# Kernel tuning notes

Measured on AMD Instinct MI355X. Metric: run time of the kernel, lower is better.

Reference implementation:

```python
import jax, jax.numpy as jnp
import numpy as np

DRUG_NUM, DIS_NUM, HIDE_DIM = 60000, 40000, 128
HOPS, N_LAYERS, N_HEADS, FFN_DIM, N_EDGES = 7, 2, 4, 512, 800000
N_NODES = DRUG_NUM + DIS_NUM


def _ln(x, s, b, eps=1e-5):
    m = jnp.mean(x, axis=-1, keepdims=True)
    v = jnp.var(x, axis=-1, keepdims=True)
    return (x - m) * jax.lax.rsqrt(v + eps) * s + b


def setup_inputs() -> dict:
    ks = jax.random.split(jax.random.key(0), 16)
    L, D, F = N_LAYERS, HIDE_DIM, FFN_DIM
    sd = 0.05  # param init scale
    n = lambda k, shape, s=sd: jax.random.normal(k, shape, jnp.float32) * s
    kk = jax.random.split(ks[15], 12)
    return {
        'ifTraining': 0,
        'uid': jax.random.randint(ks[0], (256,), 0, DRUG_NUM, jnp.int64 if jax.config.jax_enable_x64 else jnp.int32),
        'iid': jax.random.randint(ks[1], (256,), 0, DIS_NUM, jnp.int64 if jax.config.jax_enable_x64 else jnp.int32),
        'norm': 1,
        'drug_emb': n(ks[2], (DRUG_NUM, D), 0.1),
        'dis_emb': n(ks[3], (DIS_NUM, D), 0.1),
        'edge_src': jax.random.randint(ks[4], (N_EDGES,), 0, N_NODES, jnp.int32),
        'edge_dst': jax.random.randint(ks[5], (N_EDGES,), 0, N_NODES, jnp.int32),
        'edge_val': jax.random.uniform(ks[6], (N_EDGES,), jnp.float32) * 0.1,  # normalized adj values
        'att_w': n(ks[7], (D, D)), 'att_b': jnp.zeros((D,), jnp.float32),
        'ln1_s': jnp.ones((L, D), jnp.float32), 'ln1_b': jnp.zeros((L, D), jnp.float32),
        'q_w': n(kk[0], (L, D, D)), 'q_b': jnp.zeros((L, D), jnp.float32),
        'k_w': n(kk[1], (L, D, D)), 'k_b': jnp.zeros((L, D), jnp.float32),
        'v_w': n(kk[2], (L, D, D)), 'v_b': jnp.zeros((L, D), jnp.float32),
        'o_w': n(kk[3], (L, D, D)), 'o_b': jnp.zeros((L, D), jnp.float32),
        'ln2_s': jnp.ones((L, D), jnp.float32), 'ln2_b': jnp.zeros((L, D), jnp.float32),
        'f1_w': n(kk[4], (L, D, F)), 'f1_b': jnp.zeros((L, F), jnp.float32),
        'f2_w': n(kk[5], (L, F, D)), 'f2_b': jnp.zeros((L, D), jnp.float32),
        'fln_s': jnp.ones((D,), jnp.float32), 'fln_b': jnp.zeros((D,), jnp.float32),
        'attn_w': n(kk[6], (2 * D, 1)), 'attn_b': jnp.zeros((1,), jnp.float32),
    }


def reference(ifTraining, uid, iid, norm, drug_emb, dis_emb, edge_src, edge_dst, edge_val,
              att_w, att_b, ln1_s, ln1_b, q_w, q_b, k_w, k_b, v_w, v_b, o_w, o_b,
              ln2_s, ln2_b, f1_w, f1_b, f2_w, f2_b, fln_s, fln_b, attn_w, attn_b):
    N, D, S, dh = N_NODES, HIDE_DIM, HOPS + 1, HIDE_DIM // N_HEADS
    # ---- re_features: K sparse-adjacency hops over concatenated embeddings ----
    x = jnp.concatenate([drug_emb, dis_emb], axis=0)  # [N, D]
    feats = [x]
    for _ in range(HOPS):
        msgs = x[edge_src] * edge_val[:, None]          # [E, D] gather
        x = jax.ops.segment_sum(msgs, edge_dst, num_segments=N)  # [N, D] scatter-add
        feats.append(x)
    nf = jnp.stack(feats, axis=1)                        # [N, S, D]
    # ---- graph-transformer over the hop sequence (eval: dropout = identity) ----
    h = nf @ att_w + att_b                               # [N, S, D]
    for l in range(N_LAYERS):
        y = _ln(h, ln1_s[l], ln1_b[l])
        q = (y @ q_w[l] + q_b[l]).reshape(N, S, N_HEADS, dh)
        k = (y @ k_w[l] + k_b[l]).reshape(N, S, N_HEADS, dh)
        v = (y @ v_w[l] + v_b[l]).reshape(N, S, N_HEADS, dh)
        a = jnp.einsum('nshd,nthd->nhst', q, k) * (dh ** -0.5)
        a = jax.nn.softmax(a, axis=-1)                   # [N, H, S, S]
        y = jnp.einsum('nhst,nthd->nshd', a, v).reshape(N, S, D)
        h = h + (y @ o_w[l] + o_b[l])
        y = _ln(h, ln2_s[l], ln2_b[l])
        h = h + (jax.nn.gelu(y @ f1_w[l] + f1_b[l]) @ f2_w[l] + f2_b[l])
    out = _ln(h, fln_s, fln_b)
    # ---- readout: node token + softmax attention over hop tokens ----
    node = out[:, 0, :]                                  # [N, D]
    neigh = out[:, 1:, :]                                # [N, HOPS, D]
    target = jnp.broadcast_to(node[:, None, :], neigh.shape)
    att = jnp.concatenate([target, neigh], axis=-1) @ attn_w + attn_b  # [N, HOPS, 1]
    att = jax.nn.softmax(att, axis=1)
    final = node + jnp.sum(neigh * att, axis=1)          # [N, D]
    return final[:DRUG_NUM], final[DRUG_NUM:]
```

## Files before the change

### kernel.cpp

```cpp
#include <hip/hip_runtime.h>
#include <hip/hip_bf16.h>

typedef __hip_bfloat16 bf16;
typedef __attribute__((ext_vector_type(8))) short s16x8;
typedef __attribute__((ext_vector_type(4))) float f32x4;

#define NDRUG 60000
#define NDIS  40000
#define NN    100000
#define DIM   128
#define NHOPS 7
#define NEDGE 800000
#define NSB   98

__device__ __forceinline__ float u2f(unsigned short u) {
    union { unsigned int i; float f; } c; c.i = ((unsigned int)u) << 16; return c.f;
}
__device__ __forceinline__ ushort f2u(float f) {
    bf16 h = __float2bfloat16(f);
    return *reinterpret_cast<ushort*>(&h);
}


__global__ void k_init(const float* __restrict__ drug, const float* __restrict__ dis,
                       ushort* __restrict__ nf) {
    int i = blockIdx.x * 256 + threadIdx.x;
    if (i >= NN * 32) return;
    int n = i >> 5, g = (i & 31) << 2;
    const float* sp = (n < NDRUG) ? drug + (size_t)n * 128 + g
                                  : dis + (size_t)(n - NDRUG) * 128 + g;
    float4 v = *(const float4*)sp;
    ushort4 o;
    o.x = f2u(v.x); o.y = f2u(v.y); o.z = f2u(v.z); o.w = f2u(v.w);
    *(ushort4*)(nf + (size_t)n * 1024 + g) = o;
}

__global__ void k_count(const int* __restrict__ edst, int* __restrict__ cnt) {
    int e = blockIdx.x * 256 + threadIdx.x;
    if (e < NEDGE) atomicAdd(&cnt[edst[e]], 1);
}

__global__ void k_scanA(const int* __restrict__ cnt, int* __restrict__ incl,
                        int* __restrict__ btot) {
    __shared__ int part[1024];
    int b = blockIdx.x, t = threadIdx.x;
    int i = b * 1024 + t;
    part[t] = (i < NN) ? cnt[i] : 0;
    __syncthreads();
    for (int o = 1; o < 1024; o <<= 1) {
        int u = (t >= o) ? part[t - o] : 0;
        __syncthreads();
        part[t] += u;
        __syncthreads();
    }
    if (i < NN) incl[i] = part[t];
    if (t == 1023) btot[b] = part[1023];
}

__global__ void k_scanB(const int* __restrict__ btot, int* __restrict__ boff) {
    if (threadIdx.x == 0) {
        int run = 0;
        for (int b = 0; b < NSB; b++) { boff[b] = run; run += btot[b]; }
        boff[NSB] = run;
    }
}

__global__ void k_scanC(const int* __restrict__ cnt, const int* __restrict__ incl,
                        const int* __restrict__ boff, int* __restrict__ rp) {
    int i = blockIdx.x * 256 + threadIdx.x;
    if (i < NN) rp[i] = incl[i] - cnt[i] + boff[i >> 10];
    if (i == 0) rp[NN] = boff[NSB];
}

__global__ void k_copyrp(const int* __restrict__ rp, int* __restrict__ cur) {
    int i = blockIdx.x * 256 + threadIdx.x;
    if (i < NN) cur[i] = rp[i];
}

__global__ void k_scatter(const int* __restrict__ esrc, const int* __restrict__ edst,
                          const float* __restrict__ eval, int* __restrict__ cur,
                          int* __restrict__ ssrc, float* __restrict__ sval) {
    int e = blockIdx.x * 256 + threadIdx.x;
    if (e >= NEDGE) return;
    int d = edst[e];
    int pos = atomicAdd(&cur[d], 1);
    ssrc[pos] = esrc[e];
    sval[pos] = eval[e];
}

__global__ void k_hopg(ushort* __restrict__ nf, const int* __restrict__ rp,
                       const int* __restrict__ ssrc, const float* __restrict__ sval, int s) {
    int t = blockIdx.x * 256 + threadIdx.x;
    if (t >= NN * 32) return;
    int n = t >> 5, d0 = (t & 31) << 2;
    int e0 = rp[n], e1 = rp[n + 1];
    float4 a = make_float4(0.f, 0.f, 0.f, 0.f);
    for (int e = e0; e < e1; e++) {
        int src = ssrc[e];
        float val = sval[e];
        ushort4 u = *(const ushort4*)(nf + (size_t)src * 1024 + (size_t)(s - 1) * 128 + d0);
        a.x += u2f(u.x) * val; a.y += u2f(u.y) * val;
        a.z += u2f(u.z) * val; a.w += u2f(u.w) * val;
    }
    ushort4 o;
    o.x = f2u(a.x); o.y = f2u(a.y); o.z = f2u(a.z); o.w = f2u(a.w);
    *(ushort4*)(nf + (size_t)n * 1024 + (size_t)s * 128 + d0) = o;
}


__global__ void k_pack(const float* __restrict__ W, ushort* __restrict__ P, int K, int Nout) {
    int idx = blockIdx.x * 256 + threadIdx.x;
    int tot = (Nout >> 4) * (K >> 3) * 16;
    if (idx >= tot) return;
    int c = idx & 15;
    int r = idx >> 4;
    int kb = r % (K >> 3);
    int nt = r / (K >> 3);
    ushort o[8];
    #pragma unroll
    for (int i = 0; i < 8; i++)
        o[i] = f2u(W[(size_t)(kb * 8 + i) * Nout + nt * 16 + c]);
    uint4 v;
    v.x = (uint)o[0] | ((uint)o[1] << 16);
    v.y = (uint)o[2] | ((uint)o[3] << 16);
    v.z = (uint)o[4] | ((uint)o[5] << 16);
    v.w = (uint)o[6] | ((uint)o[7] << 16);
    *(uint4*)(P + (size_t)idx * 8) = v;
}

__global__ void k_catb(const float* __restrict__ qb, const float* __restrict__ kb,
                       const float* __restrict__ vb, float* __restrict__ o) {
    int i = threadIdx.x;
    o[i] = (i < 128) ? qb[i] : ((i < 256) ? kb[i - 128] : vb[i - 256]);
}


template <int ACT, int ADD, int OUTBF, int NTPW>
__global__ void k_mgemm(const ushort* __restrict__ X, const ushort* __restrict__ Wp,
                        const float* __restrict__ bias, void* __restrict__ Yv,
                        int M, int K, int Nout) {
    int w = threadIdx.x >> 6, lane = threadIdx.x & 63;
    int lr = lane & 15, lg = lane >> 4;
    int m0 = blockIdx.x * 16;
    int kb8 = K >> 3;
    int row = m0 + lr; if (row > M - 1) row = M - 1;
    const ushort* ap = X + (size_t)row * K + lg * 8;
    f32x4 acc[NTPW] = {};
    for (int k0 = 0; k0 < K; k0 += 32, ap += 32) {
        s16x8 af = *(const s16x8*)ap;
        int kb = (k0 >> 3) + lg;
        #pragma unroll
        for (int t = 0; t < NTPW; t++) {
            int nt = w + t * 4;
            const ushort* bp = Wp + (((size_t)nt * kb8 + kb) * 16 + lr) * 8;
            s16x8 bf_ = *(const s16x8*)bp;
            acc[t] = __builtin_amdgcn_mfma_f32_16x16x32_bf16(af, bf_, acc[t], 0, 0, 0);
        }
    }
    #pragma unroll
    for (int t = 0; t < NTPW; t++) {
        int n = (w + t * 4) * 16 + lr;
        float bv = bias[n];
        #pragma unroll
        for (int j = 0; j < 4; j++) {
            int m = m0 + lg * 4 + j;
            if (m >= M) continue;
            float v = acc[t][j] + bv;
            if (ACT == 1) {
                float x = v;
                float z = 0.7978845608028654f * (x + 0.044715f * x * x * x);
                v = x / (1.0f + __expf(-2.0f * z));
            }
            if (OUTBF) {
                ((ushort*)Yv)[(size_t)m * Nout + n] = f2u(v);
            } else if (ADD) {
                ((float*)Yv)[(size_t)m * Nout + n] += v;
            } else {
                ((float*)Yv)[(size_t)m * Nout + n] = v;
            }
        }
    }
}


__global__ void k_layer(float* __restrict__ H,
                        const ushort* __restrict__ Wqkv, const ushort* __restrict__ Wo,
                        const ushort* __restrict__ Wf1, const ushort* __restrict__ Wf2,
                        const float* __restrict__ s1v, const float* __restrict__ b1v,
                        const float* __restrict__ bqkv, const float* __restrict__ bo,
                        const float* __restrict__ s2v, const float* __restrict__ b2v,
                        const float* __restrict__ bf1, const float* __restrict__ bf2,
                        int M) {
    __shared__ float  h[16][132];
    __shared__ ushort ylds[16][136];
    __shared__ ushort big[16][520];
    __shared__ float  as_[2][256];
    int tid = threadIdx.x;
    int w = tid >> 6, lane = tid & 63;
    int lr = lane & 15, lg = lane >> 4;
    int m0 = blockIdx.x * 16;

    #pragma unroll
    for (int i = 0; i < 2; i++) {
        int gi = i * 256 + tid;
        int row = gi >> 5, c4 = (gi & 31) << 2;
        int grow = m0 + row; if (grow > M - 1) grow = M - 1;
        *(float4*)&h[row][c4] = *(const float4*)(H + (size_t)grow * 128 + c4);
    }
    __syncthreads();

    #pragma unroll
    for (int i = 0; i < 4; i++) {
        int row = w * 4 + i;
        float2 x = *(const float2*)&h[row][lane * 2];
        float sum = x.x + x.y, sq = x.x * x.x + x.y * x.y;
        #pragma unroll
        for (int o = 32; o; o >>= 1) { sum += __shfl_xor(sum, o); sq += __shfl_xor(sq, o); }
        float mean = sum * (1.f / 128.f);
        float inv = rsqrtf(sq * (1.f / 128.f) - mean * mean + 1e-5f);
        float y0 = (x.x - mean) * inv * s1v[lane * 2 + 0] + b1v[lane * 2 + 0];
        float y1 = (x.y - mean) * inv * s1v[lane * 2 + 1] + b1v[lane * 2 + 1];
        *(uint*)&ylds[row][lane * 2] = (uint)f2u(y0) | ((uint)f2u(y1) << 16);
    }
    __syncthreads();

    {
        f32x4 acc[6] = {};
        for (int k0 = 0; k0 < 128; k0 += 32) {
            s16x8 af = *(const s16x8*)&ylds[lr][lg * 8 + k0];
            int kb = (k0 >> 3) + lg;
            #pragma unroll
            for (int t = 0; t < 6; t++) {
                int nt = w + t * 4;
                const ushort* bp = Wqkv + (((size_t)nt * 16 + kb) * 16 + lr) * 8;
                s16x8 bf_ = *(const s16x8*)bp;
                acc[t] = __builtin_amdgcn_mfma_f32_16x16x32_bf16(af, bf_, acc[t], 0, 0, 0);
            }
        }
        #pragma unroll
        for (int t = 0; t < 6; t++) {
            int n = (w + t * 4) * 16 + lr;
            float bv = bqkv[n];
            #pragma unroll
            for (int j = 0; j < 4; j++) big[lg * 4 + j][n] = f2u(acc[t][j] + bv);
        }
    }
    __syncthreads();

    if (w < 2) {
        int hh = lane >> 4, s_ = (lane >> 1) & 7, p = lane & 1;
        const float scale = 0.17677669529663687f;
        float dots[4];
        float mx = -1e30f;
        #pragma unroll
        for (int t4 = 0; t4 < 4; t4++) {
            int t = p * 4 + t4;
            float dot = 0.f;
            #pragma unroll
            for (int d = 0; d < 32; d++)
                dot += u2f(big[w * 8 + s_][hh * 32 + d]) * u2f(big[w * 8 + t][128 + hh * 32 + d]);
            dots[t4] = dot * scale;
            mx = fmaxf(mx, dots[t4]);
        }
        mx = fmaxf(mx, __shfl_xor(mx, 1));
        float sum = 0.f, e4[4];
        #pragma unroll
        for (int t4 = 0; t4 < 4; t4++) { e4[t4] = __expf(dots[t4] - mx); sum += e4[t4]; }
        sum += __shfl_xor(sum, 1);
        float rinv = 1.f / sum;
        #pragma unroll
        for (int t4 = 0; t4 < 4; t4++) as_[w][hh * 64 + s_ * 8 + p * 4 + t4] = e4[t4] * rinv;
    }
    __syncthreads();

    if (w < 2) {
        #pragma unroll
        for (int i = 0; i < 16; i++) {
            int o = i * 64 + lane;
            int ss = o >> 7, rem = o & 127, h2 = rem >> 5, dd = rem & 31;
            float accv = 0.f;
            #pragma unroll
            for (int t = 0; t < 8; t++)
                accv += as_[w][h2 * 64 + ss * 8 + t] * u2f(big[w * 8 + t][256 + h2 * 32 + dd]);
            ylds[w * 8 + ss][rem] = f2u(accv);
        }
    }
    __syncthreads();

    {
        f32x4 acc[2] = {};
        for (int k0 = 0; k0 < 128; k0 += 32) {
            s16x8 af = *(const s16x8*)&ylds[lr][lg * 8 + k0];
            int kb = (k0 >> 3) + lg;
            #pragma unroll
            for (int t = 0; t < 2; t++) {
                int nt = w + t * 4;
                const ushort* bp = Wo + (((size_t)nt * 16 + kb) * 16 + lr) * 8;
                s16x8 bf_ = *(const s16x8*)bp;
                acc[t] = __builtin_amdgcn_mfma_f32_16x16x32_bf16(af, bf_, acc[t], 0, 0, 0);
            }
        }
        #pragma unroll
        for (int t = 0; t < 2; t++) {
            int n = (w + t * 4) * 16 + lr;
            float bv = bo[n];
            #pragma unroll
            for (int j = 0; j < 4; j++) h[lg * 4 + j][n] += acc[t][j] + bv;
        }
    }
    __syncthreads();

    #pragma unroll
    for (int i = 0; i < 4; i++) {
        int row = w * 4 + i;
        float2 x = *(const float2*)&h[row][lane * 2];
        float sum = x.x + x.y, sq = x.x * x.x + x.y * x.y;
        #pragma unroll
        for (int o = 32; o; o >>= 1) { sum += __shfl_xor(sum, o); sq += __shfl_xor(sq, o); }
        float mean = sum * (1.f / 128.f);
        float inv = rsqrtf(sq * (1.f / 128.f) - mean * mean + 1e-5f);
        float y0 = (x.x - mean) * inv * s2v[lane * 2 + 0] + b2v[lane * 2 + 0];
        float y1 = (x.y - mean) * inv * s2v[lane * 2 + 1] + b2v[lane * 2 + 1];
        *(uint*)&ylds[row][lane * 2] = (uint)f2u(y0) | ((uint)f2u(y1) << 16);
    }
    __syncthreads();

    {
        f32x4 acc[8] = {};
        for (int k0 = 0; k0 < 128; k0 += 32) {
            s16x8 af = *(const s16x8*)&ylds[lr][lg * 8 + k0];
            int kb = (k0 >> 3) + lg;
            #pragma unroll
            for (int t = 0; t < 8; t++) {
                int nt = w + t * 4;
                const ushort* bp = Wf1 + (((size_t)nt * 16 + kb) * 16 + lr) * 8;
                s16x8 bf_ = *(const s16x8*)bp;
                acc[t] = __builtin_amdgcn_mfma_f32_16x16x32_bf16(af, bf_, acc[t], 0, 0, 0);
            }
        }
        #pragma unroll
        for (int t = 0; t < 8; t++) {
            int n = (w + t * 4) * 16 + lr;
            float bv = bf1[n];
            #pragma unroll
            for (int j = 0; j < 4; j++) {
                float x = acc[t][j] + bv;
                float z = 0.7978845608028654f * (x + 0.044715f * x * x * x);
                big[lg * 4 + j][n] = f2u(x / (1.0f + __expf(-2.0f * z)));
            }
        }
    }
    __syncthreads();

    {
        f32x4 acc[2] = {};
        for (int k0 = 0; k0 < 512; k0 += 32) {
            s16x8 af = *(const s16x8*)&big[lr][lg * 8 + k0];
            int kb = (k0 >> 3) + lg;
            #pragma unroll
            for (int t = 0; t < 2; t++) {
                int nt = w + t * 4;
                const ushort* bp = Wf2 + (((size_t)nt * 64 + kb) * 16 + lr) * 8;
                s16x8 bf_ = *(const s16x8*)bp;
                acc[t] = __builtin_amdgcn_mfma_f32_16x16x32_bf16(af, bf_, acc[t], 0, 0, 0);
            }
        }
        #pragma unroll
        for (int t = 0; t < 2; t++) {
            int n = (w + t * 4) * 16 + lr;
            float bv = bf2[n];
            #pragma unroll
            for (int j = 0; j < 4; j++) h[lg * 4 + j][n] += acc[t][j] + bv;
        }
    }
    __syncthreads();

    #pragma unroll
    for (int i = 0; i < 2; i++) {
        int gi = i * 256 + tid;
        int row = gi >> 5, c4 = (gi & 31) << 2;
        int grow = m0 + row;
        if (grow < M) *(float4*)(H + (size_t)grow * 128 + c4) = *(const float4*)&h[row][c4];
    }
}


__global__ void k_pool(const float* __restrict__ Hc, const float* __restrict__ fs,
                       const float* __restrict__ fb, const float* __restrict__ aw,
                       const float* __restrict__ ab, float* __restrict__ out,
                       int Nc, int n0g) {
    int w = threadIdx.x >> 6, lane = threadIdx.x & 63;
    int nl = blockIdx.x * 4 + w;
    if (nl >= Nc) return;
    const float* hp = Hc + (size_t)nl * 1024;
    float s0 = fs[lane * 2], s1 = fs[lane * 2 + 1];
    float b0 = fb[lane * 2], b1 = fb[lane * 2 + 1];
    float2 yl[8];
    #pragma unroll
    for (int s = 0; s < 8; s++) {
        float2 x = *(const float2*)(hp + s * DIM + lane * 2);
        float sum = x.x + x.y, sq = x.x * x.x + x.y * x.y;
        #pragma unroll
        for (int o = 32; o; o >>= 1) { sum += __shfl_xor(sum, o); sq += __shfl_xor(sq, o); }
        float mean = sum * (1.f / 128.f);
        float inv = rsqrtf(sq * (1.f / 128.f) - mean * mean + 1e-5f);
        yl[s].x = (x.x - mean) * inv * s0 + b0;
        yl[s].y = (x.y - mean) * inv * s1 + b1;
    }
    float awn0 = aw[lane * 2], awn1 = aw[lane * 2 + 1];
    float awh0 = aw[128 + lane * 2], awh1 = aw[128 + lane * 2 + 1];
    float abv = ab[0];
    float lg[7];
    #pragma unroll
    for (int s = 0; s < 7; s++) {
        float part = yl[0].x * awn0 + yl[0].y * awn1 + yl[s + 1].x * awh0 + yl[s + 1].y * awh1;
        #pragma unroll
        for (int o = 32; o; o >>= 1) part += __shfl_xor(part, o);
        lg[s] = part + abv;
    }
    float mx = lg[0];
    #pragma unroll
    for (int s = 1; s < 7; s++) mx = fmaxf(mx, lg[s]);
    float sum = 0.f;
    #pragma unroll
    for (int s = 0; s < 7; s++) { lg[s] = __expf(lg[s] - mx); sum += lg[s]; }
    float rinv = 1.f / sum;
    float2 f = yl[0];
    #pragma unroll
    for (int s = 0; s < 7; s++) { f.x += lg[s] * rinv * yl[s + 1].x; f.y += lg[s] * rinv * yl[s + 1].y; }
    size_t ob = (size_t)(n0g + nl) * DIM + lane * 2;
    out[ob + 0] = f.x;
    out[ob + 1] = f.y;
}


extern "C" void kernel_launch(void* const* d_in, const int* in_sizes, int n_in,
                              void* d_out, int out_size, void* d_ws, size_t ws_size,
                              hipStream_t stream) {
    const float* drug  = (const float*)d_in[4];
    const float* dis   = (const float*)d_in[5];
    const int*   esrc  = (const int*)d_in[6];
    const int*   edst  = (const int*)d_in[7];
    const float* eval  = (const float*)d_in[8];
    const float* att_w = (const float*)d_in[9];
    const float* att_b = (const float*)d_in[10];
    const float* ln1_s = (const float*)d_in[11];
    const float* ln1_b = (const float*)d_in[12];
    const float* q_w   = (const float*)d_in[13];
    const float* q_b   = (const float*)d_in[14];
    const float* k_w   = (const float*)d_in[15];
    const float* k_b   = (const float*)d_in[16];
    const float* v_w   = (const float*)d_in[17];
    const float* v_b   = (const float*)d_in[18];
    const float* o_w   = (const float*)d_in[19];
    const float* o_b   = (const float*)d_in[20];
    const float* ln2_s = (const float*)d_in[21];
    const float* ln2_b = (const float*)d_in[22];
    const float* f1_w  = (const float*)d_in[23];
    const float* f1_b  = (const float*)d_in[24];
    const float* f2_w  = (const float*)d_in[25];
    const float* f2_b  = (const float*)d_in[26];
    const float* fln_s = (const float*)d_in[27];
    const float* fln_b = (const float*)d_in[28];
    const float* aw    = (const float*)d_in[29];
    const float* ab    = (const float*)d_in[30];
    float* out = (float*)d_out;

    char* ws = (char*)d_ws;
    size_t nfB = (size_t)NN * 1024 * 2;
    ushort* nf = (ushort*)ws;
    size_t off = (nfB + 255) & ~(size_t)255;

    ushort* wpk = (ushort*)(ws + off);
    size_t offCsr = off + (1 << 20);
    int*   rp   = (int*)(ws + offCsr);
    int*   cnt  = rp + (NN + 1);
    int*   ssrc = cnt + NN;
    float* sval = (float*)(ssrc + NEDGE);
    int*   incl = (int*)(sval + NEDGE);
    int*   btot = incl + NN;
    int*   boff = btot + 128;
    size_t csrInts = (size_t)(NN + 1) + NN + NEDGE + NEDGE + NN + 256;
    size_t off2 = offCsr + ((csrInts * 4 + 255) & ~(size_t)255);

    size_t scratchB = (ws_size > off2) ? ws_size - off2 : 0;
    long long ncMax = (long long)(scratchB / 4096);
    ncMax &= ~1LL;
    if (ncMax < 2) ncMax = 2;
    int Nc = (int)((ncMax < NN) ? ncMax : NN);
    int nchunks = (NN + Nc - 1) / Nc;
    Nc = (NN + nchunks - 1) / nchunks;
    if (Nc & 1) Nc++;
    float* hbuf = (float*)(ws + off2);

    size_t wpAtt = 0;
    size_t wpQKV[2], wpO[2], wpF1[2], wpF2[2];
    {
        size_t p = 16384;
        for (int l = 0; l < 2; l++) {
            wpQKV[l] = p; p += 49152;
            wpO[l]   = p; p += 16384;
            wpF1[l]  = p; p += 65536;
            wpF2[l]  = p; p += 65536;
        }
    }
    float* qkvB = (float*)(wpk + 409600);

    {
        int b128 = (16384 / 8 + 255) / 256;
        int b512 = (65536 / 8 + 255) / 256;
        k_pack<<<b128, 256, 0, stream>>>(att_w, wpk + wpAtt, 128, 128);
        for (int l = 0; l < 2; l++) {
            k_pack<<<b128, 256, 0, stream>>>(q_w + (size_t)l * 16384, wpk + wpQKV[l], 128, 128);
            k_pack<<<b128, 256, 0, stream>>>(k_w + (size_t)l * 16384, wpk + wpQKV[l] + 16384, 128, 128);
            k_pack<<<b128, 256, 0, stream>>>(v_w + (size_t)l * 16384, wpk + wpQKV[l] + 32768, 128, 128);
            k_pack<<<b128, 256, 0, stream>>>(o_w + (size_t)l * 16384, wpk + wpO[l], 128, 128);
            k_pack<<<b512, 256, 0, stream>>>(f1_w + (size_t)l * 65536, wpk + wpF1[l], 128, 512);
            k_pack<<<b512, 256, 0, stream>>>(f2_w + (size_t)l * 65536, wpk + wpF2[l], 512, 128);
            k_catb<<<1, 384, 0, stream>>>(q_b + l * 128, k_b + l * 128, v_b + l * 128, qkvB + l * 384);
        }
    }

    (void)hipMemsetAsync(cnt, 0, (size_t)NN * 4, stream);
    k_count<<<(NEDGE + 255) / 256, 256, 0, stream>>>(edst, cnt);
    k_scanA<<<NSB, 1024, 0, stream>>>(cnt, incl, btot);
    k_scanB<<<1, 64, 0, stream>>>(btot, boff);
    k_scanC<<<(NN + 255) / 256, 256, 0, stream>>>(cnt, incl, boff, rp);
    k_copyrp<<<(NN + 255) / 256, 256, 0, stream>>>(rp, cnt);
    k_scatter<<<(NEDGE + 255) / 256, 256, 0, stream>>>(esrc, edst, eval, cnt, ssrc, sval);

    k_init<<<(NN * 32 + 255) / 256, 256, 0, stream>>>(drug, dis, nf);
    for (int s = 1; s <= NHOPS; s++)
        k_hopg<<<(NN * 32 + 255) / 256, 256, 0, stream>>>(nf, rp, ssrc, sval, s);

    for (int c = 0; c < nchunks; c++) {
        int cn0 = c * Nc;
        int cn = NN - cn0; if (cn > Nc) cn = Nc;
        if (cn <= 0) break;
        int Mc = cn * 8;
        int mb = (Mc + 15) / 16;
        int nb = (cn + 3) / 4;

        k_mgemm<0, 0, 0, 2><<<mb, 256, 0, stream>>>(nf + (size_t)cn0 * 1024, wpk + wpAtt,
                                                    att_b, hbuf, Mc, 128, 128);
        for (int l = 0; l < 2; l++) {
            k_layer<<<mb, 256, 0, stream>>>(hbuf, wpk + wpQKV[l], wpk + wpO[l],
                                            wpk + wpF1[l], wpk + wpF2[l],
                                            ln1_s + l * 128, ln1_b + l * 128,
                                            qkvB + l * 384, o_b + l * 128,
                                            ln2_s + l * 128, ln2_b + l * 128,
                                            f1_b + l * 512, f2_b + l * 128, Mc);
        }
        k_pool<<<nb, 256, 0, stream>>>(hbuf, fln_s, fln_b, aw, ab, out, cn, cn0);
    }
    (void)in_sizes; (void)n_in; (void)out_size;
}
```

Baseline: 2.957 ms.

## Fuse both transformer layers into one kernel keeping activations in LDS

Merges the two per-layer k_layer launches into a single k_layer2 kernel that loops over both layers while the 16-row h tile stays in shared memory. This removes one fp32 global write and read of the hidden state per chunk, plus one launch. It also spreads the attention-times-V step across all four waves instead of two. The weight pack offsets are recomputed as fixed layer strides.

```diff
diff --git a/kernel.cpp b/kernel.cpp
--- a/kernel.cpp
+++ b/kernel.cpp
@@ -183,14 +183,13 @@
 }
 
 
-__global__ void k_layer(float* __restrict__ H,
-                        const ushort* __restrict__ Wqkv, const ushort* __restrict__ Wo,
-                        const ushort* __restrict__ Wf1, const ushort* __restrict__ Wf2,
-                        const float* __restrict__ s1v, const float* __restrict__ b1v,
-                        const float* __restrict__ bqkv, const float* __restrict__ bo,
-                        const float* __restrict__ s2v, const float* __restrict__ b2v,
-                        const float* __restrict__ bf1, const float* __restrict__ bf2,
-                        int M) {
+__global__ void k_layer2(float* __restrict__ H, const ushort* __restrict__ wpk,
+                         const float* __restrict__ qkvB,
+                         const float* __restrict__ ln1_s, const float* __restrict__ ln1_b,
+                         const float* __restrict__ o_b,
+                         const float* __restrict__ ln2_s, const float* __restrict__ ln2_b,
+                         const float* __restrict__ f1_b, const float* __restrict__ f2_b,
+                         int M) {
     __shared__ float  h[16][132];
     __shared__ ushort ylds[16][136];
     __shared__ ushort big[16][520];
@@ -209,171 +208,187 @@
     }
     __syncthreads();
 
-    #pragma unroll
-    for (int i = 0; i < 4; i++) {
-        int row = w * 4 + i;
-        float2 x = *(const float2*)&h[row][lane * 2];
-        float sum = x.x + x.y, sq = x.x * x.x + x.y * x.y;
+    for (int l = 0; l < 2; l++) {
+        const ushort* Wqkv = wpk + 16384  + (size_t)l * 196608;
+        const ushort* Wo   = wpk + 65536  + (size_t)l * 196608;
+        const ushort* Wf1  = wpk + 81920  + (size_t)l * 196608;
+        const ushort* Wf2  = wpk + 147456 + (size_t)l * 196608;
+        const float* s1v = ln1_s + l * 128;
+        const float* b1v = ln1_b + l * 128;
+        const float* bqkv = qkvB + l * 384;
+        const float* bo  = o_b + l * 128;
+        const float* s2v = ln2_s + l * 128;
+        const float* b2v = ln2_b + l * 128;
+        const float* bf1 = f1_b + l * 512;
+        const float* bf2 = f2_b + l * 128;
+
         #pragma unroll
-        for (int o = 32; o; o >>= 1) { sum += __shfl_xor(sum, o); sq += __shfl_xor(sq, o); }
-        float mean = sum * (1.f / 128.f);
-        float inv = rsqrtf(sq * (1.f / 128.f) - mean * mean + 1e-5f);
-        float y0 = (x.x - mean) * inv * s1v[lane * 2 + 0] + b1v[lane * 2 + 0];
-        float y1 = (x.y - mean) * inv * s1v[lane * 2 + 1] + b1v[lane * 2 + 1];
-        *(uint*)&ylds[row][lane * 2] = (uint)f2u(y0) | ((uint)f2u(y1) << 16);
-    }
-    __syncthreads();
-
-    {
-        f32x4 acc[6] = {};
-        for (int k0 = 0; k0 < 128; k0 += 32) {
-            s16x8 af = *(const s16x8*)&ylds[lr][lg * 8 + k0];
-            int kb = (k0 >> 3) + lg;
+        for (int i = 0; i < 4; i++) {
+            int row = w * 4 + i;
+            float2 x = *(const float2*)&h[row][lane * 2];
+            float sum = x.x + x.y, sq = x.x * x.x + x.y * x.y;
+            #pragma unroll
+            for (int o = 32; o; o >>= 1) { sum += __shfl_xor(sum, o); sq += __shfl_xor(sq, o); }
+            float mean = sum * (1.f / 128.f);
+            float inv = rsqrtf(sq * (1.f / 128.f) - mean * mean + 1e-5f);
+            float y0 = (x.x - mean) * inv * s1v[lane * 2 + 0] + b1v[lane * 2 + 0];
+            float y1 = (x.y - mean) * inv * s1v[lane * 2 + 1] + b1v[lane * 2 + 1];
+            *(uint*)&ylds[row][lane * 2] = (uint)f2u(y0) | ((uint)f2u(y1) << 16);
+        }
+        __syncthreads();
+
+        {
+            f32x4 acc[6] = {};
+            for (int k0 = 0; k0 < 128; k0 += 32) {
+                s16x8 af = *(const s16x8*)&ylds[lr][lg * 8 + k0];
+                int kb = (k0 >> 3) + lg;
+                #pragma unroll
+                for (int t = 0; t < 6; t++) {
+                    int nt = w + t * 4;
+                    const ushort* bp = Wqkv + (((size_t)nt * 16 + kb) * 16 + lr) * 8;
+                    s16x8 bf_ = *(const s16x8*)bp;
+                    acc[t] = __builtin_amdgcn_mfma_f32_16x16x32_bf16(af, bf_, acc[t], 0, 0, 0);
+                }
+            }
             #pragma unroll
             for (int t = 0; t < 6; t++) {
-                int nt = w + t * 4;
-                const ushort* bp = Wqkv + (((size_t)nt * 16 + kb) * 16 + lr) * 8;
-                s16x8 bf_ = *(const s16x8*)bp;
-                acc[t] = __builtin_amdgcn_mfma_f32_16x16x32_bf16(af, bf_, acc[t], 0, 0, 0);
-            }
-        }
+                int n = (w + t * 4) * 16 + lr;
+                float bv = bqkv[n];
+                #pragma unroll
+                for (int j = 0; j < 4; j++) big[lg * 4 + j][n] = f2u(acc[t][j] + bv);
+            }
+        }
+        __syncthreads();
+
+        if (w < 2) {
+            int hh = lane >> 4, s_ = (lane >> 1) & 7, p = lane & 1;
+            const float scale = 0.17677669529663687f;
+            float dots[4];
+            float mx = -1e30f;
+            #pragma unroll
+            for (int t4 = 0; t4 < 4; t4++) {
+                int t = p * 4 + t4;
+                float dot = 0.f;
+                #pragma unroll
+                for (int d = 0; d < 32; d++)
+                    dot += u2f(big[w * 8 + s_][hh * 32 + d]) * u2f(big[w * 8 + t][128 + hh * 32 + d]);
+                dots[t4] = dot * scale;
+                mx = fmaxf(mx, dots[t4]);
+            }
+            mx = fmaxf(mx, __shfl_xor(mx, 1));
+            float sum = 0.f, e4[4];
+            #pragma unroll
+            for (int t4 = 0; t4 < 4; t4++) { e4[t4] = __expf(dots[t4] - mx); sum += e4[t4]; }
+            sum += __shfl_xor(sum, 1);
+            float rinv = 1.f / sum;
+            #pragma unroll
+            for (int t4 = 0; t4 < 4; t4++) as_[w][hh * 64 + s_ * 8 + p * 4 + t4] = e4[t4] * rinv;
+        }
+        __syncthreads();
+
+        {
+            int nd = w & 1, hf = w >> 1;
+            #pragma unroll
+            for (int i = 0; i < 8; i++) {
+                int o = hf * 512 + i * 64 + lane;
+                int ss = o >> 7, rem = o & 127, h2 = rem >> 5, dd = rem & 31;
+                float accv = 0.f;
+                #pragma unroll
+                for (int t = 0; t < 8; t++)
+                    accv += as_[nd][h2 * 64 + ss * 8 + t] * u2f(big[nd * 8 + t][256 + h2 * 32 + dd]);
+                ylds[nd * 8 + ss][rem] = f2u(accv);
+            }
+        }
+        __syncthreads();
+
+        {
+            f32x4 acc[2] = {};
+            for (int k0 = 0; k0 < 128; k0 += 32) {
+                s16x8 af = *(const s16x8*)&ylds[lr][lg * 8 + k0];
+                int kb = (k0 >> 3) + lg;
+                #pragma unroll
+                for (int t = 0; t < 2; t++) {
+                    int nt = w + t * 4;
+                    const ushort* bp = Wo + (((size_t)nt * 16 + kb) * 16 + lr) * 8;
+                    s16x8 bf_ = *(const s16x8*)bp;
+                    acc[t] = __builtin_amdgcn_mfma_f32_16x16x32_bf16(af, bf_, acc[t], 0, 0, 0);
+                }
+            }
+            #pragma unroll
+            for (int t = 0; t < 2; t++) {
+                int n = (w + t * 4) * 16 + lr;
+                float bv = bo[n];
+                #pragma unroll
+                for (int j = 0; j < 4; j++) h[lg * 4 + j][n] += acc[t][j] + bv;
+            }
+        }
+        __syncthreads();
+
         #pragma unroll
-        for (int t = 0; t < 6; t++) {
-            int n = (w + t * 4) * 16 + lr;
-            float bv = bqkv[n];
-            #pragma unroll
-            for (int j = 0; j < 4; j++) big[lg * 4 + j][n] = f2u(acc[t][j] + bv);
-        }
-    }
-    __syncthreads();
-
-    if (w < 2) {
-        int hh = lane >> 4, s_ = (lane >> 1) & 7, p = lane & 1;
-        const float scale = 0.17677669529663687f;
-        float dots[4];
-        float mx = -1e30f;
-        #pragma unroll
-        for (int t4 = 0; t4 < 4; t4++) {
-            int t = p * 4 + t4;
-            float dot = 0.f;
-            #pragma unroll
-            for (int d = 0; d < 32; d++)
-                dot += u2f(big[w * 8 + s_][hh * 32 + d]) * u2f(big[w * 8 + t][128 + hh * 32 + d]);
-            dots[t4] = dot * scale;
-            mx = fmaxf(mx, dots[t4]);
-        }
-        mx = fmaxf(mx, __shfl_xor(mx, 1));
-        float sum = 0.f, e4[4];
-        #pragma unroll
-        for (int t4 = 0; t4 < 4; t4++) { e4[t4] = __expf(dots[t4] - mx); sum += e4[t4]; }
-        sum += __shfl_xor(sum, 1);
-        float rinv = 1.f / sum;
-        #pragma unroll
-        for (int t4 = 0; t4 < 4; t4++) as_[w][hh * 64 + s_ * 8 + p * 4 + t4] = e4[t4] * rinv;
-    }
-    __syncthreads();
-
-    if (w < 2) {
-        #pragma unroll
-        for (int i = 0; i < 16; i++) {
-            int o = i * 64 + lane;
-            int ss = o >> 7, rem = o & 127, h2 = rem >> 5, dd = rem & 31;
-            float accv = 0.f;
-            #pragma unroll
-            for (int t = 0; t < 8; t++)
-                accv += as_[w][h2 * 64 + ss * 8 + t] * u2f(big[w * 8 + t][256 + h2 * 32 + dd]);
-            ylds[w * 8 + ss][rem] = f2u(accv);
-        }
-    }
-    __syncthreads();
-
-    {
-        f32x4 acc[2] = {};
-        for (int k0 = 0; k0 < 128; k0 += 32) {
-            s16x8 af = *(const s16x8*)&ylds[lr][lg * 8 + k0];
-            int kb = (k0 >> 3) + lg;
+        for (int i = 0; i < 4; i++) {
+            int row = w * 4 + i;
+            float2 x = *(const float2*)&h[row][lane * 2];
+            float sum = x.x + x.y, sq = x.x * x.x + x.y * x.y;
+            #pragma unroll
+            for (int o = 32; o; o >>= 1) { sum += __shfl_xor(sum, o); sq += __shfl_xor(sq, o); }
+            float mean = sum * (1.f / 128.f);
+            float inv = rsqrtf(sq * (1.f / 128.f) - mean * mean + 1e-5f);
+            float y0 = (x.x - mean) * inv * s2v[lane * 2 + 0] + b2v[lane * 2 + 0];
+            float y1 = (x.y - mean) * inv * s2v[lane * 2 + 1] + b2v[lane * 2 + 1];
+            *(uint*)&ylds[row][lane * 2] = (uint)f2u(y0) | ((uint)f2u(y1) << 16);
+        }
+        __syncthreads();
+
+        {
+            f32x4 acc[8] = {};
+            for (int k0 = 0; k0 < 128; k0 += 32) {
+                s16x8 af = *(const s16x8*)&ylds[lr][lg * 8 + k0];
+                int kb = (k0 >> 3) + lg;
+                #pragma unroll
+                for (int t = 0; t < 8; t++) {
+                    int nt = w + t * 4;
+                    const ushort* bp = Wf1 + (((size_t)nt * 16 + kb) * 16 + lr) * 8;
+                    s16x8 bf_ = *(const s16x8*)bp;
+                    acc[t] = __builtin_amdgcn_mfma_f32_16x16x32_bf16(af, bf_, acc[t], 0, 0, 0);
+                }
+            }
+            #pragma unroll
+            for (int t = 0; t < 8; t++) {
+                int n = (w + t * 4) * 16 + lr;
+                float bv = bf1[n];
+                #pragma unroll
+                for (int j = 0; j < 4; j++) {
+                    float x = acc[t][j] + bv;
+                    float z = 0.7978845608028654f * (x + 0.044715f * x * x * x);
+                    big[lg * 4 + j][n] = f2u(x / (1.0f + __expf(-2.0f * z)));
+                }
+            }
+        }
+        __syncthreads();
+
+        {
+            f32x4 acc[2] = {};
+            for (int k0 = 0; k0 < 512; k0 += 32) {
+                s16x8 af = *(const s16x8*)&big[lr][lg * 8 + k0];
+                int kb = (k0 >> 3) + lg;
+                #pragma unroll
+                for (int t = 0; t < 2; t++) {
+                    int nt = w + t * 4;
+                    const ushort* bp = Wf2 + (((size_t)nt * 64 + kb) * 16 + lr) * 8;
+                    s16x8 bf_ = *(const s16x8*)bp;
+                    acc[t] = __builtin_amdgcn_mfma_f32_16x16x32_bf16(af, bf_, acc[t], 0, 0, 0);
+                }
+            }
             #pragma unroll
             for (int t = 0; t < 2; t++) {
-                int nt = w + t * 4;
-                const ushort* bp = Wo + (((size_t)nt * 16 + kb) * 16 + lr) * 8;
-                s16x8 bf_ = *(const s16x8*)bp;
-                acc[t] = __builtin_amdgcn_mfma_f32_16x16x32_bf16(af, bf_, acc[t], 0, 0, 0);
-            }
-        }
-        #pragma unroll
-        for (int t = 0; t < 2; t++) {
-            int n = (w + t * 4) * 16 + lr;
-            float bv = bo[n];
-            #pragma unroll
-            for (int j = 0; j < 4; j++) h[lg * 4 + j][n] += acc[t][j] + bv;
-        }
-    }
-    __syncthreads();
-
-    #pragma unroll
-    for (int i = 0; i < 4; i++) {
-        int row = w * 4 + i;
-        float2 x = *(const float2*)&h[row][lane * 2];
-        float sum = x.x + x.y, sq = x.x * x.x + x.y * x.y;
-        #pragma unroll
-        for (int o = 32; o; o >>= 1) { sum += __shfl_xor(sum, o); sq += __shfl_xor(sq, o); }
-        float mean = sum * (1.f / 128.f);
-        float inv = rsqrtf(sq * (1.f / 128.f) - mean * mean + 1e-5f);
-        float y0 = (x.x - mean) * inv * s2v[lane * 2 + 0] + b2v[lane * 2 + 0];
-        float y1 = (x.y - mean) * inv * s2v[lane * 2 + 1] + b2v[lane * 2 + 1];
-        *(uint*)&ylds[row][lane * 2] = (uint)f2u(y0) | ((uint)f2u(y1) << 16);
-    }
-    __syncthreads();
-
-    {
-        f32x4 acc[8] = {};
-        for (int k0 = 0; k0 < 128; k0 += 32) {
-            s16x8 af = *(const s16x8*)&ylds[lr][lg * 8 + k0];
-            int kb = (k0 >> 3) + lg;
-            #pragma unroll
-            for (int t = 0; t < 8; t++) {
-                int nt = w + t * 4;
-                const ushort* bp = Wf1 + (((size_t)nt * 16 + kb) * 16 + lr) * 8;
-                s16x8 bf_ = *(const s16x8*)bp;
-                acc[t] = __builtin_amdgcn_mfma_f32_16x16x32_bf16(af, bf_, acc[t], 0, 0, 0);
-            }
-        }
-        #pragma unroll
-        for (int t = 0; t < 8; t++) {
-            int n = (w + t * 4) * 16 + lr;
-            float bv = bf1[n];
-            #pragma unroll
-            for (int j = 0; j < 4; j++) {
-                float x = acc[t][j] + bv;
-                float z = 0.7978845608028654f * (x + 0.044715f * x * x * x);
-                big[lg * 4 + j][n] = f2u(x / (1.0f + __expf(-2.0f * z)));
-            }
-        }
-    }
-    __syncthreads();
-
-    {
-        f32x4 acc[2] = {};
-        for (int k0 = 0; k0 < 512; k0 += 32) {
-            s16x8 af = *(const s16x8*)&big[lr][lg * 8 + k0];
-            int kb = (k0 >> 3) + lg;
-            #pragma unroll
-            for (int t = 0; t < 2; t++) {
-                int nt = w + t * 4;
-                const ushort* bp = Wf2 + (((size_t)nt * 64 + kb) * 16 + lr) * 8;
-                s16x8 bf_ = *(const s16x8*)bp;
-                acc[t] = __builtin_amdgcn_mfma_f32_16x16x32_bf16(af, bf_, acc[t], 0, 0, 0);
-            }
-        }
-        #pragma unroll
-        for (int t = 0; t < 2; t++) {
-            int n = (w + t * 4) * 16 + lr;
-            float bv = bf2[n];
-            #pragma unroll
-            for (int j = 0; j < 4; j++) h[lg * 4 + j][n] += acc[t][j] + bv;
-        }
-    }
-    __syncthreads();
+                int n = (w + t * 4) * 16 + lr;
+                float bv = bf2[n];
+                #pragma unroll
+                for (int j = 0; j < 4; j++) h[lg * 4 + j][n] += acc[t][j] + bv;
+            }
+        }
+        __syncthreads();
+    }
 
     #pragma unroll
     for (int i = 0; i < 2; i++) {
@@ -493,30 +508,20 @@
     if (Nc & 1) Nc++;
     float* hbuf = (float*)(ws + off2);
 
-    size_t wpAtt = 0;
-    size_t wpQKV[2], wpO[2], wpF1[2], wpF2[2];
-    {
-        size_t p = 16384;
-        for (int l = 0; l < 2; l++) {
-            wpQKV[l] = p; p += 49152;
-            wpO[l]   = p; p += 16384;
-            wpF1[l]  = p; p += 65536;
-            wpF2[l]  = p; p += 65536;
-        }
-    }
     float* qkvB = (float*)(wpk + 409600);
 
     {
         int b128 = (16384 / 8 + 255) / 256;
         int b512 = (65536 / 8 + 255) / 256;
-        k_pack<<<b128, 256, 0, stream>>>(att_w, wpk + wpAtt, 128, 128);
+        k_pack<<<b128, 256, 0, stream>>>(att_w, wpk, 128, 128);
         for (int l = 0; l < 2; l++) {
-            k_pack<<<b128, 256, 0, stream>>>(q_w + (size_t)l * 16384, wpk + wpQKV[l], 128, 128);
-            k_pack<<<b128, 256, 0, stream>>>(k_w + (size_t)l * 16384, wpk + wpQKV[l] + 16384, 128, 128);
-            k_pack<<<b128, 256, 0, stream>>>(v_w + (size_t)l * 16384, wpk + wpQKV[l] + 32768, 128, 128);
-            k_pack<<<b128, 256, 0, stream>>>(o_w + (size_t)l * 16384, wpk + wpO[l], 128, 128);
-            k_pack<<<b512, 256, 0, stream>>>(f1_w + (size_t)l * 65536, wpk + wpF1[l], 128, 512);
-            k_pack<<<b512, 256, 0, stream>>>(f2_w + (size_t)l * 65536, wpk + wpF2[l], 512, 128);
+            size_t base = 16384 + (size_t)l * 196608;
+            k_pack<<<b128, 256, 0, stream>>>(q_w + (size_t)l * 16384, wpk + base, 128, 128);
+            k_pack<<<b128, 256, 0, stream>>>(k_w + (size_t)l * 16384, wpk + base + 16384, 128, 128);
+            k_pack<<<b128, 256, 0, stream>>>(v_w + (size_t)l * 16384, wpk + base + 32768, 128, 128);
+            k_pack<<<b128, 256, 0, stream>>>(o_w + (size_t)l * 16384, wpk + base + 49152, 128, 128);
+            k_pack<<<b512, 256, 0, stream>>>(f1_w + (size_t)l * 65536, wpk + base + 65536, 128, 512);
+            k_pack<<<b512, 256, 0, stream>>>(f2_w + (size_t)l * 65536, wpk + base + 131072, 512, 128);
             k_catb<<<1, 384, 0, stream>>>(q_b + l * 128, k_b + l * 128, v_b + l * 128, qkvB + l * 384);
         }
     }
@@ -541,16 +546,10 @@
         int mb = (Mc + 15) / 16;
         int nb = (cn + 3) / 4;
 
-        k_mgemm<0, 0, 0, 2><<<mb, 256, 0, stream>>>(nf + (size_t)cn0 * 1024, wpk + wpAtt,
+        k_mgemm<0, 0, 0, 2><<<mb, 256, 0, stream>>>(nf + (size_t)cn0 * 1024, wpk,
                                                     att_b, hbuf, Mc, 128, 128);
-        for (int l = 0; l < 2; l++) {
-            k_layer<<<mb, 256, 0, stream>>>(hbuf, wpk + wpQKV[l], wpk + wpO[l],
-                                            wpk + wpF1[l], wpk + wpF2[l],
-                                            ln1_s + l * 128, ln1_b + l * 128,
-                                            qkvB + l * 384, o_b + l * 128,
-                                            ln2_s + l * 128, ln2_b + l * 128,
-                                            f1_b + l * 512, f2_b + l * 128, Mc);
-        }
+        k_layer2<<<mb, 256, 0, stream>>>(hbuf, wpk, qkvB, ln1_s, ln1_b, o_b,
+                                         ln2_s, ln2_b, f1_b, f2_b, Mc);
         k_pool<<<nb, 256, 0, stream>>>(hbuf, fln_s, fln_b, aw, ab, out, cn, cn0);
     }
     (void)in_sizes; (void)n_in; (void)out_size;
```

Result: slower. 6.587 ms (+122.8%).

## Process 32 rows per block in fused transformer layer kernel

Applied to the files above, without the earlier changes.

The fused layer kernel now handles 32 token rows (4 nodes) per block instead of 16, with each wave issuing two MFMA row fragments that share each loaded weight fragment. Weight traffic from global/L2 per row is halved and all four waves now take part in attention instead of two. The FFN1 stage is split into two passes to limit accumulator register pressure. LDS use per block doubles, which may lower occupancy, and the chunk size is rounded to a multiple of four nodes.

```diff
diff --git a/kernel.cpp b/kernel.cpp
--- a/kernel.cpp
+++ b/kernel.cpp
@@ -191,17 +191,17 @@
                         const float* __restrict__ s2v, const float* __restrict__ b2v,
                         const float* __restrict__ bf1, const float* __restrict__ bf2,
                         int M) {
-    __shared__ float  h[16][132];
-    __shared__ ushort ylds[16][136];
-    __shared__ ushort big[16][520];
-    __shared__ float  as_[2][256];
+    __shared__ float  h[32][132];
+    __shared__ ushort ylds[32][136];
+    __shared__ ushort big[32][520];
+    __shared__ float  as_[4][256];
     int tid = threadIdx.x;
     int w = tid >> 6, lane = tid & 63;
     int lr = lane & 15, lg = lane >> 4;
-    int m0 = blockIdx.x * 16;
-
-    #pragma unroll
-    for (int i = 0; i < 2; i++) {
+    int m0 = blockIdx.x * 32;
+
+    #pragma unroll
+    for (int i = 0; i < 4; i++) {
         int gi = i * 256 + tid;
         int row = gi >> 5, c4 = (gi & 31) << 2;
         int grow = m0 + row; if (grow > M - 1) grow = M - 1;
@@ -210,8 +210,8 @@
     __syncthreads();
 
     #pragma unroll
-    for (int i = 0; i < 4; i++) {
-        int row = w * 4 + i;
+    for (int i = 0; i < 8; i++) {
+        int row = w * 8 + i;
         float2 x = *(const float2*)&h[row][lane * 2];
         float sum = x.x + x.y, sq = x.x * x.x + x.y * x.y;
         #pragma unroll
@@ -225,16 +225,18 @@
     __syncthreads();
 
     {
-        f32x4 acc[6] = {};
+        f32x4 acc[2][6] = {};
         for (int k0 = 0; k0 < 128; k0 += 32) {
-            s16x8 af = *(const s16x8*)&ylds[lr][lg * 8 + k0];
+            s16x8 af0 = *(const s16x8*)&ylds[lr][lg * 8 + k0];
+            s16x8 af1 = *(const s16x8*)&ylds[16 + lr][lg * 8 + k0];
             int kb = (k0 >> 3) + lg;
             #pragma unroll
             for (int t = 0; t < 6; t++) {
                 int nt = w + t * 4;
                 const ushort* bp = Wqkv + (((size_t)nt * 16 + kb) * 16 + lr) * 8;
                 s16x8 bf_ = *(const s16x8*)bp;
-                acc[t] = __builtin_amdgcn_mfma_f32_16x16x32_bf16(af, bf_, acc[t], 0, 0, 0);
+                acc[0][t] = __builtin_amdgcn_mfma_f32_16x16x32_bf16(af0, bf_, acc[0][t], 0, 0, 0);
+                acc[1][t] = __builtin_amdgcn_mfma_f32_16x16x32_bf16(af1, bf_, acc[1][t], 0, 0, 0);
             }
         }
         #pragma unroll
@@ -242,12 +244,15 @@
             int n = (w + t * 4) * 16 + lr;
             float bv = bqkv[n];
             #pragma unroll
-            for (int j = 0; j < 4; j++) big[lg * 4 + j][n] = f2u(acc[t][j] + bv);
-        }
-    }
-    __syncthreads();
-
-    if (w < 2) {
+            for (int rf = 0; rf < 2; rf++)
+                #pragma unroll
+                for (int j = 0; j < 4; j++)
+                    big[rf * 16 + lg * 4 + j][n] = f2u(acc[rf][t][j] + bv);
+        }
+    }
+    __syncthreads();
+
+    {
         int hh = lane >> 4, s_ = (lane >> 1) & 7, p = lane & 1;
         const float scale = 0.17677669529663687f;
         float dots[4];
@@ -273,7 +278,7 @@
     }
     __syncthreads();
 
-    if (w < 2) {
+    {
         #pragma unroll
         for (int i = 0; i < 16; i++) {
             int o = i * 64 + lane;
@@ -288,16 +293,18 @@
     __syncthreads();
 
     {
-        f32x4 acc[2] = {};
+        f32x4 acc[2][2] = {};
         for (int k0 = 0; k0 < 128; k0 += 32) {
-            s16x8 af = *(const s16x8*)&ylds[lr][lg * 8 + k0];
+            s16x8 af0 = *(const s16x8*)&ylds[lr][lg * 8 + k0];
+            s16x8 af1 = *(const s16x8*)&ylds[16 + lr][lg * 8 + k0];
             int kb = (k0 >> 3) + lg;
             #pragma unroll
             for (int t = 0; t < 2; t++) {
                 int nt = w + t * 4;
                 const ushort* bp = Wo + (((size_t)nt * 16 + kb) * 16 + lr) * 8;
                 s16x8 bf_ = *(const s16x8*)bp;
-                acc[t] = __builtin_amdgcn_mfma_f32_16x16x32_bf16(af, bf_, acc[t], 0, 0, 0);
+                acc[0][t] = __builtin_amdgcn_mfma_f32_16x16x32_bf16(af0, bf_, acc[0][t], 0, 0, 0);
+                acc[1][t] = __builtin_amdgcn_mfma_f32_16x16x32_bf16(af1, bf_, acc[1][t], 0, 0, 0);
             }
         }
         #pragma unroll
@@ -305,14 +312,17 @@
             int n = (w + t * 4) * 16 + lr;
             float bv = bo[n];
             #pragma unroll
-            for (int j = 0; j < 4; j++) h[lg * 4 + j][n] += acc[t][j] + bv;
-        }
-    }
-    __syncthreads();
-
-    #pragma unroll
-    for (int i = 0; i < 4; i++) {
-        int row = w * 4 + i;
+            for (int rf = 0; rf < 2; rf++)
+                #pragma unroll
+                for (int j = 0; j < 4; j++)
+                    h[rf * 16 + lg * 4 + j][n] += acc[rf][t][j] + bv;
+        }
+    }
+    __syncthreads();
+
+    #pragma unroll
+    for (int i = 0; i < 8; i++) {
+        int row = w * 8 + i;
         float2 x = *(const float2*)&h[row][lane * 2];
         float sum = x.x + x.y, sq = x.x * x.x + x.y * x.y;
         #pragma unroll
@@ -325,44 +335,51 @@
     }
     __syncthreads();
 
-    {
-        f32x4 acc[8] = {};
+    #pragma unroll
+    for (int ps = 0; ps < 2; ps++) {
+        f32x4 acc[2][4] = {};
         for (int k0 = 0; k0 < 128; k0 += 32) {
-            s16x8 af = *(const s16x8*)&ylds[lr][lg * 8 + k0];
+            s16x8 af0 = *(const s16x8*)&ylds[lr][lg * 8 + k0];
+            s16x8 af1 = *(const s16x8*)&ylds[16 + lr][lg * 8 + k0];
             int kb = (k0 >> 3) + lg;
             #pragma unroll
-            for (int t = 0; t < 8; t++) {
-                int nt = w + t * 4;
+            for (int t = 0; t < 4; t++) {
+                int nt = w + (ps * 4 + t) * 4;
                 const ushort* bp = Wf1 + (((size_t)nt * 16 + kb) * 16 + lr) * 8;
                 s16x8 bf_ = *(const s16x8*)bp;
-                acc[t] = __builtin_amdgcn_mfma_f32_16x16x32_bf16(af, bf_, acc[t], 0, 0, 0);
+                acc[0][t] = __builtin_amdgcn_mfma_f32_16x16x32_bf16(af0, bf_, acc[0][t], 0, 0, 0);
+                acc[1][t] = __builtin_amdgcn_mfma_f32_16x16x32_bf16(af1, bf_, acc[1][t], 0, 0, 0);
             }
         }
         #pragma unroll
-        for (int t = 0; t < 8; t++) {
-            int n = (w + t * 4) * 16 + lr;
+        for (int t = 0; t < 4; t++) {
+            int n = (w + (ps * 4 + t) * 4) * 16 + lr;
             float bv = bf1[n];
             #pragma unroll
-            for (int j = 0; j < 4; j++) {
-                float x = acc[t][j] + bv;
-                float z = 0.7978845608028654f * (x + 0.044715f * x * x * x);
-                big[lg * 4 + j][n] = f2u(x / (1.0f + __expf(-2.0f * z)));
-            }
-        }
-    }
-    __syncthreads();
-
-    {
-        f32x4 acc[2] = {};
+            for (int rf = 0; rf < 2; rf++)
+                #pragma unroll
+                for (int j = 0; j < 4; j++) {
+                    float x = acc[rf][t][j] + bv;
+                    float z = 0.7978845608028654f * (x + 0.044715f * x * x * x);
+                    big[rf * 16 + lg * 4 + j][n] = f2u(x / (1.0f + __expf(-2.0f * z)));
+                }
+        }
+    }
+    __syncthreads();
+
+    {
+        f32x4 acc[2][2] = {};
         for (int k0 = 0; k0 < 512; k0 += 32) {
-            s16x8 af = *(const s16x8*)&big[lr][lg * 8 + k0];
+            s16x8 af0 = *(const s16x8*)&big[lr][lg * 8 + k0];
+            s16x8 af1 = *(const s16x8*)&big[16 + lr][lg * 8 + k0];
             int kb = (k0 >> 3) + lg;
             #pragma unroll
             for (int t = 0; t < 2; t++) {
                 int nt = w + t * 4;
                 const ushort* bp = Wf2 + (((size_t)nt * 64 + kb) * 16 + lr) * 8;
                 s16x8 bf_ = *(const s16x8*)bp;
-                acc[t] = __builtin_amdgcn_mfma_f32_16x16x32_bf16(af, bf_, acc[t], 0, 0, 0);
+                acc[0][t] = __builtin_amdgcn_mfma_f32_16x16x32_bf16(af0, bf_, acc[0][t], 0, 0, 0);
+                acc[1][t] = __builtin_amdgcn_mfma_f32_16x16x32_bf16(af1, bf_, acc[1][t], 0, 0, 0);
             }
         }
         #pragma unroll
@@ -370,13 +387,16 @@
             int n = (w + t * 4) * 16 + lr;
             float bv = bf2[n];
             #pragma unroll
-            for (int j = 0; j < 4; j++) h[lg * 4 + j][n] += acc[t][j] + bv;
-        }
-    }
-    __syncthreads();
-
-    #pragma unroll
-    for (int i = 0; i < 2; i++) {
+            for (int rf = 0; rf < 2; rf++)
+                #pragma unroll
+                for (int j = 0; j < 4; j++)
+                    h[rf * 16 + lg * 4 + j][n] += acc[rf][t][j] + bv;
+        }
+    }
+    __syncthreads();
+
+    #pragma unroll
+    for (int i = 0; i < 4; i++) {
         int gi = i * 256 + tid;
         int row = gi >> 5, c4 = (gi & 31) << 2;
         int grow = m0 + row;
@@ -485,12 +505,12 @@
 
     size_t scratchB = (ws_size > off2) ? ws_size - off2 : 0;
     long long ncMax = (long long)(scratchB / 4096);
-    ncMax &= ~1LL;
-    if (ncMax < 2) ncMax = 2;
+    ncMax &= ~3LL;
+    if (ncMax < 4) ncMax = 4;
     int Nc = (int)((ncMax < NN) ? ncMax : NN);
     int nchunks = (NN + Nc - 1) / Nc;
     Nc = (NN + nchunks - 1) / nchunks;
-    if (Nc & 1) Nc++;
+    Nc = (Nc + 3) & ~3;
     float* hbuf = (float*)(ws + off2);
 
     size_t wpAtt = 0;
@@ -538,18 +558,19 @@
         int cn = NN - cn0; if (cn > Nc) cn = Nc;
         if (cn <= 0) break;
         int Mc = cn * 8;
-        int mb = (Mc + 15) / 16;
+        int mb16 = (Mc + 15) / 16;
+        int mb32 = (Mc + 31) / 32;
         int nb = (cn + 3) / 4;
 
-        k_mgemm<0, 0, 0, 2><<<mb, 256, 0, stream>>>(nf + (size_t)cn0 * 1024, wpk + wpAtt,
-                                                    att_b, hbuf, Mc, 128, 128);
+        k_mgemm<0, 0, 0, 2><<<mb16, 256, 0, stream>>>(nf + (size_t)cn0 * 1024, wpk + wpAtt,
+                                                      att_b, hbuf, Mc, 128, 128);
         for (int l = 0; l < 2; l++) {
-            k_layer<<<mb, 256, 0, stream>>>(hbuf, wpk + wpQKV[l], wpk + wpO[l],
-                                            wpk + wpF1[l], wpk + wpF2[l],
-                                            ln1_s + l * 128, ln1_b + l * 128,
-                                            qkvB + l * 384, o_b + l * 128,
-                                            ln2_s + l * 128, ln2_b + l * 128,
-                                            f1_b + l * 512, f2_b + l * 128, Mc);
+            k_layer<<<mb32, 256, 0, stream>>>(hbuf, wpk + wpQKV[l], wpk + wpO[l],
+                                              wpk + wpF1[l], wpk + wpF2[l],
+                                              ln1_s + l * 128, ln1_b + l * 128,
+                                              qkvB + l * 384, o_b + l * 128,
+                                              ln2_s + l * 128, ln2_b + l * 128,
+                                              f1_b + l * 512, f2_b + l * 128, Mc);
         }
         k_pool<<<nb, 256, 0, stream>>>(hbuf, fln_s, fln_b, aw, ab, out, cn, cn0);
     }
```

New measurement: 4.449 ms. 50.5% more time.
